# Kernel optimization log

Hardware: AMD Instinct MI355X
Metric: run time of the kernel (lower is better)

## Reference

```python
import jax, jax.numpy as jnp
import numpy as np

N_NODES = 50000
N_EDGES = 800000
IN_C, HID_C, OUT_C = 64, 128, 64


def setup_inputs() -> dict:
    key = jax.random.key(0)
    k0, k1, k2, k3 = jax.random.split(key, 4)
    x = jax.random.normal(k0, (N_NODES, IN_C), dtype=jnp.float32)
    edge_index = jax.random.randint(k1, (2, N_EDGES), 0, N_NODES, dtype=jnp.int64)
    # Glorot-ish init for the two GCNConv linear weights
    W1 = jax.random.normal(k2, (IN_C, HID_C), dtype=jnp.float32) * (1.0 / np.sqrt(IN_C))
    b1 = jnp.zeros((HID_C,), dtype=jnp.float32)
    W2 = jax.random.normal(k3, (HID_C, OUT_C), dtype=jnp.float32) * (1.0 / np.sqrt(HID_C))
    b2 = jnp.zeros((OUT_C,), dtype=jnp.float32)
    return {"x": x, "edge_index": edge_index, "W1": W1, "b1": b1, "W2": W2, "b2": b2}


def _gcn_conv(x, src, dst, norm, W, b, n_nodes):
    # GCNConv: out = D^{-1/2} (A+I) D^{-1/2} (x W) + b
    xw = x @ W                              # [N, out_c]
    msg = xw[src] * norm[:, None]           # [E+N, out_c] gather + scale
    agg = jax.ops.segment_sum(msg, dst, num_segments=n_nodes)  # scatter-add
    return agg + b


def reference(x, edge_index, W1, b1, W2, b2):
    n = x.shape[0]
    loops = jnp.arange(n, dtype=edge_index.dtype)
    src = jnp.concatenate([edge_index[0], loops])  # add self-loops
    dst = jnp.concatenate([edge_index[1], loops])
    # symmetric normalization over A + I
    deg = jax.ops.segment_sum(jnp.ones_like(dst, dtype=x.dtype), dst, num_segments=n)
    dinv = jnp.where(deg > 0, jax.lax.rsqrt(jnp.maximum(deg, 1.0)), 0.0)
    norm = dinv[src] * dinv[dst]
    h = jax.nn.relu(_gcn_conv(x, src, dst, norm, W1, b1, n))
    return _gcn_conv(h, src, dst, norm, W2, b2, n)
```

## Files before the change

### kernel.cpp

```cpp
#include <hip/hip_runtime.h>
#include <cstdint>


#define IN_C 64
#define HID_C 128
#define OUT_C 64
#define CH 2048
#define CAP 8192

typedef short bf16x8 __attribute__((ext_vector_type(8)));
typedef float f32x4 __attribute__((ext_vector_type(4)));

__device__ __forceinline__ unsigned int f2bf(float f) {
    unsigned int u = __float_as_uint(f);
    return (u + 0x7FFFu + ((u >> 16) & 1u)) >> 16;
}
__device__ __forceinline__ float bf2f(unsigned int hi16) {
    return __uint_as_float(hi16 << 16);
}

__device__ __forceinline__ int edge_val(const void* ei, long long idx, int is64) {
    if (is64) return (int)((const long long*)ei)[idx];
    return ((const int*)ei)[idx];
}

__global__ __launch_bounds__(256) void init_conv_k(const unsigned int* __restrict__ ei,
                                                   int* __restrict__ flag,
                                                   int* __restrict__ bcur,
                                                   const float4* __restrict__ x4,
                                                   uint2* __restrict__ xbf2, int NC4) {
    int i = blockIdx.x * 256 + threadIdx.x;
    if (i < NC4) {
        float4 v = x4[i];
        uint2 o;
        o.x = f2bf(v.x) | (f2bf(v.y) << 16);
        o.y = f2bf(v.z) | (f2bf(v.w) << 16);
        xbf2[i] = o;
    }
    if (blockIdx.x == 0) bcur[threadIdx.x] = threadIdx.x * CAP;
    if (i == 0) {
        int is64 = 1;
#pragma unroll
        for (int k = 0; k < 16; ++k) is64 &= (ei[2 * k + 1] == 0u) ? 1 : 0;
        *flag = is64;
    }
}

__global__ __launch_bounds__(256) void partition_k(const void* __restrict__ ei, int E,
                                                   const int* __restrict__ flag,
                                                   int* __restrict__ bcur,
                                                   int2* __restrict__ tmp) {
    __shared__ int2 stage[CH];
    __shared__ int hist[256];
    __shared__ int off[256];
    __shared__ int rcur[256];
    __shared__ int goff[256];
    __shared__ int wsum[4];
    const int tid = threadIdx.x;
    const int base = blockIdx.x * CH;
    const int cnt = min(CH, E - base);
    const int is64 = *flag;
    hist[tid] = 0;
    __syncthreads();
    int sa[CH / 256], da[CH / 256];
    int ne = 0;
#pragma unroll
    for (int k = 0; k < CH / 256; ++k) {
        int i = tid + k * 256;
        if (i < cnt) {
            sa[ne] = edge_val(ei, base + i, is64);
            da[ne] = edge_val(ei, (long long)E + base + i, is64);
            ne++;
        }
    }
    for (int k = 0; k < ne; ++k) atomicAdd(&hist[da[k] >> 8], 1);
    __syncthreads();
    {
        int v = hist[tid];
        int lane = tid & 63, wid = tid >> 6;
        int s = v;
#pragma unroll
        for (int o = 1; o < 64; o <<= 1) {
            int t = __shfl_up(s, o, 64);
            if (lane >= o) s += t;
        }
        if (lane == 63) wsum[wid] = s;
        __syncthreads();
        int w = 0;
#pragma unroll
        for (int j = 0; j < 4; ++j)
            if (j < wid) w += wsum[j];
        off[tid] = w + s - v;
        rcur[tid] = w + s - v;
    }
    __syncthreads();
    for (int k = 0; k < ne; ++k) {
        int b = da[k] >> 8;
        int r = atomicAdd(&rcur[b], 1);
        stage[r] = make_int2(sa[k], da[k]);
    }
    __syncthreads();
    {
        int c = hist[tid];
        goff[tid] = (c > 0) ? atomicAdd(&bcur[tid], c) : 0;
    }
    __syncthreads();
    for (int i = tid; i < cnt; i += 256) {
        int2 e = stage[i];
        int b = e.y >> 8;
        tmp[goff[b] + (i - off[b])] = e;
    }
}

__global__ __launch_bounds__(256) void finalize_k(const int2* __restrict__ tmp,
                                                  const int* __restrict__ bcur,
                                                  int* __restrict__ rowptr,
                                                  float* __restrict__ dinv,
                                                  int* __restrict__ edata,
                                                  int N, int E) {
    __shared__ int cnt[256];
    __shared__ int cur[256];
    __shared__ int sc[256];
    __shared__ int wsum[4];
    const int tid = threadIdx.x;
    const int bid = blockIdx.x;
    const int node0 = bid << 8;
    const int lane = tid & 63, wid = tid >> 6;
    {
        int v = bcur[tid] - tid * CAP;
        int s = v;
#pragma unroll
        for (int o = 1; o < 64; o <<= 1) {
            int t = __shfl_up(s, o, 64);
            if (lane >= o) s += t;
        }
        if (lane == 63) wsum[wid] = s;
        cnt[tid] = 0;
        __syncthreads();
        int w = 0;
#pragma unroll
        for (int j = 0; j < 4; ++j)
            if (j < wid) w += wsum[j];
        sc[tid] = w + s - v;
    }
    __syncthreads();
    const int base = bid * CAP;
    const int end = bcur[bid];
    for (int i = base + tid; i < end; i += 256)
        atomicAdd(&cnt[tmp[i].y - node0], 1);
    __syncthreads();
    const int gi = node0 + tid;
    int v = cnt[tid];
    if (gi < N) dinv[gi] = rsqrtf((float)(v + 1));
    int s = v;
#pragma unroll
    for (int o = 1; o < 64; o <<= 1) {
        int t = __shfl_up(s, o, 64);
        if (lane >= o) s += t;
    }
    if (lane == 63) wsum[wid] = s;
    __syncthreads();
    int w = 0;
#pragma unroll
    for (int j = 0; j < 4; ++j)
        if (j < wid) w += wsum[j];
    int rp = sc[bid] + w + s - v;
    if (gi < N) rowptr[gi] = rp;
    cur[tid] = rp;
    if (bid == 0 && tid == 0) rowptr[N] = E;
    __syncthreads();
    for (int i = base + tid; i < end; i += 256) {
        int2 e = tmp[i];
        int pos = atomicAdd(&cur[e.y - node0], 1);
        edata[pos] = e.x;
    }
}

template <bool BIAS, bool OBF>
__global__ __launch_bounds__(256) void aggregate_bf16_k(const uint4* __restrict__ feat4,
                                                        const int* __restrict__ rowptr,
                                                        const int* __restrict__ edata,
                                                        const float* __restrict__ dinv,
                                                        const float4* __restrict__ bias4,
                                                        void* __restrict__ outp, int N) {
    const int tid = threadIdx.x;
    const int node = blockIdx.x * 32 + (tid >> 3);
    const int t = tid & 7;
    if (node >= N) return;
    float dn = dinv[node];
    float sl = dn * dn;
    uint4 sv = feat4[(size_t)node * 8 + t];
    float acc[8];
    acc[0] = bf2f(sv.x & 0xFFFF) * sl;
    acc[1] = bf2f(sv.x >> 16) * sl;
    acc[2] = bf2f(sv.y & 0xFFFF) * sl;
    acc[3] = bf2f(sv.y >> 16) * sl;
    acc[4] = bf2f(sv.z & 0xFFFF) * sl;
    acc[5] = bf2f(sv.z >> 16) * sl;
    acc[6] = bf2f(sv.w & 0xFFFF) * sl;
    acc[7] = bf2f(sv.w >> 16) * sl;
    int e = rowptr[node];
    const int e1 = rowptr[node + 1];
#define ACC_EDGE(V, W)                                  \
    acc[0] = fmaf((W), bf2f((V).x & 0xFFFF), acc[0]);   \
    acc[1] = fmaf((W), bf2f((V).x >> 16), acc[1]);      \
    acc[2] = fmaf((W), bf2f((V).y & 0xFFFF), acc[2]);   \
    acc[3] = fmaf((W), bf2f((V).y >> 16), acc[3]);      \
    acc[4] = fmaf((W), bf2f((V).z & 0xFFFF), acc[4]);   \
    acc[5] = fmaf((W), bf2f((V).z >> 16), acc[5]);      \
    acc[6] = fmaf((W), bf2f((V).w & 0xFFFF), acc[6]);   \
    acc[7] = fmaf((W), bf2f((V).w >> 16), acc[7]);
    for (; e + 4 <= e1; e += 4) {
        int s0 = edata[e], s1 = edata[e + 1], s2 = edata[e + 2], s3 = edata[e + 3];
        float w0 = dinv[s0] * dn, w1 = dinv[s1] * dn;
        float w2 = dinv[s2] * dn, w3 = dinv[s3] * dn;
        uint4 f0 = feat4[(size_t)s0 * 8 + t];
        uint4 f1 = feat4[(size_t)s1 * 8 + t];
        uint4 f2 = feat4[(size_t)s2 * 8 + t];
        uint4 f3 = feat4[(size_t)s3 * 8 + t];
        ACC_EDGE(f0, w0);
        ACC_EDGE(f1, w1);
        ACC_EDGE(f2, w2);
        ACC_EDGE(f3, w3);
    }
    for (; e < e1; ++e) {
        int s0 = edata[e];
        float w0 = dinv[s0] * dn;
        uint4 f0 = feat4[(size_t)s0 * 8 + t];
        ACC_EDGE(f0, w0);
    }
#undef ACC_EDGE
    if (BIAS) {
        float4 b0 = bias4[2 * t], b1v = bias4[2 * t + 1];
        acc[0] += b0.x; acc[1] += b0.y; acc[2] += b0.z; acc[3] += b0.w;
        acc[4] += b1v.x; acc[5] += b1v.y; acc[6] += b1v.z; acc[7] += b1v.w;
    }
    if (OBF) {
        uint4 o;
        o.x = f2bf(acc[0]) | (f2bf(acc[1]) << 16);
        o.y = f2bf(acc[2]) | (f2bf(acc[3]) << 16);
        o.z = f2bf(acc[4]) | (f2bf(acc[5]) << 16);
        o.w = f2bf(acc[6]) | (f2bf(acc[7]) << 16);
        ((uint4*)outp)[(size_t)node * 8 + t] = o;
    } else {
        float4* out4 = (float4*)outp;
        out4[(size_t)node * 16 + 2 * t] = make_float4(acc[0], acc[1], acc[2], acc[3]);
        out4[(size_t)node * 16 + 2 * t + 1] = make_float4(acc[4], acc[5], acc[6], acc[7]);
    }
}

__global__ __launch_bounds__(256) void gemm1_mfma_k(const uint4* __restrict__ A8,
                                                    const float* __restrict__ W1,
                                                    const float* __restrict__ b1,
                                                    unsigned short* __restrict__ h, int M) {
    __shared__ uint4 As[64 * 8];
    __shared__ unsigned short BsU[128 * 64];
    const int tid = threadIdx.x;
    const int node0 = blockIdx.x * 64;
    for (int i = tid; i < 64 * 8; i += 256) {
        int r = i >> 3, c = i & 7;
        uint4 v = make_uint4(0u, 0u, 0u, 0u);
        if (node0 + r < M) v = A8[(size_t)(node0 + r) * 8 + c];
        As[r * 8 + (c ^ (r & 7))] = v;
    }
    {
        const float4* W4 = (const float4*)W1;
        for (int i = tid; i < 64 * 32; i += 256) {
            int k = i >> 5, n4 = i & 31;
            float4 v = W4[i];
            int n = n4 * 4;
#pragma unroll
            for (int j = 0; j < 4; ++j) {
                float f = (j == 0) ? v.x : (j == 1) ? v.y : (j == 2) ? v.z : v.w;
                int nn = n + j;
                int chunk = k >> 3;
                BsU[nn * 64 + ((chunk ^ (nn & 7)) << 3) + (k & 7)] =
                    (unsigned short)f2bf(f);
            }
        }
    }
    __syncthreads();

    const int lane = tid & 63;
    const int wv = tid >> 6;
    const int lr = lane & 15;
    const int lk = lane >> 4;
    f32x4 acc[4][2];
#pragma unroll
    for (int mt = 0; mt < 4; ++mt)
#pragma unroll
        for (int nb = 0; nb < 2; ++nb) acc[mt][nb] = (f32x4){0.f, 0.f, 0.f, 0.f};

#pragma unroll
    for (int ks = 0; ks < 2; ++ks) {
        bf16x8 a[4], b[2];
#pragma unroll
        for (int mt = 0; mt < 4; ++mt) {
            int r = mt * 16 + lr;
            int chunk = ks * 4 + lk;
            a[mt] = __builtin_bit_cast(bf16x8, As[r * 8 + (chunk ^ (r & 7))]);
        }
#pragma unroll
        for (int nb = 0; nb < 2; ++nb) {
            int n = wv * 32 + nb * 16 + lr;
            int chunk = ks * 4 + lk;
            b[nb] = __builtin_bit_cast(
                bf16x8, ((const uint4*)(BsU + n * 64))[chunk ^ (n & 7)]);
        }
#pragma unroll
        for (int mt = 0; mt < 4; ++mt)
#pragma unroll
            for (int nb = 0; nb < 2; ++nb)
                acc[mt][nb] = __builtin_amdgcn_mfma_f32_16x16x32_bf16(
                    a[mt], b[nb], acc[mt][nb], 0, 0, 0);
    }
#pragma unroll
    for (int nb = 0; nb < 2; ++nb) {
        int col = wv * 32 + nb * 16 + lr;
        float bb = b1[col];
#pragma unroll
        for (int mt = 0; mt < 4; ++mt) {
#pragma unroll
            for (int j = 0; j < 4; ++j) {
                int row = node0 + mt * 16 + (lane >> 4) * 4 + j;
                if (row < M) {
                    float v = fmaxf(acc[mt][nb][j] + bb, 0.f);
                    h[(size_t)row * HID_C + col] = (unsigned short)f2bf(v);
                }
            }
        }
    }
}

__global__ __launch_bounds__(256) void gemm2_mfma_k(const uint4* __restrict__ A16,
                                                    const float* __restrict__ W2,
                                                    unsigned short* __restrict__ hwb, int M) {
    __shared__ uint4 As[64 * 16];
    __shared__ unsigned short BsU[64 * 128];
    const int tid = threadIdx.x;
    const int node0 = blockIdx.x * 64;
    for (int i = tid; i < 64 * 16; i += 256) {
        int r = i >> 4, c = i & 15;
        uint4 v = make_uint4(0u, 0u, 0u, 0u);
        if (node0 + r < M) v = A16[(size_t)(node0 + r) * 16 + c];
        As[r * 16 + (c ^ (r & 7))] = v;
    }
    {
        const float4* W4 = (const float4*)W2;
        for (int i = tid; i < 128 * 16; i += 256) {
            int k = i >> 4, n4 = i & 15;
            float4 v = W4[i];
            int n = n4 * 4;
#pragma unroll
            for (int j = 0; j < 4; ++j) {
                float f = (j == 0) ? v.x : (j == 1) ? v.y : (j == 2) ? v.z : v.w;
                int nn = n + j;
                int chunk = k >> 3;
                BsU[nn * 128 + ((chunk ^ (nn & 7)) << 3) + (k & 7)] =
                    (unsigned short)f2bf(f);
            }
        }
    }
    __syncthreads();

    const int lane = tid & 63;
    const int wv = tid >> 6;
    const int lr = lane & 15;
    const int lk = lane >> 4;
    f32x4 acc[4];
#pragma unroll
    for (int mt = 0; mt < 4; ++mt) acc[mt] = (f32x4){0.f, 0.f, 0.f, 0.f};

#pragma unroll
    for (int ks = 0; ks < 4; ++ks) {
        bf16x8 a[4], b;
        int chunk = ks * 4 + lk;
#pragma unroll
        for (int mt = 0; mt < 4; ++mt) {
            int r = mt * 16 + lr;
            a[mt] = __builtin_bit_cast(bf16x8, As[r * 16 + (chunk ^ (r & 7))]);
        }
        {
            int n = wv * 16 + lr;
            b = __builtin_bit_cast(
                bf16x8, ((const uint4*)(BsU + n * 128))[chunk ^ (n & 7)]);
        }
#pragma unroll
        for (int mt = 0; mt < 4; ++mt)
            acc[mt] = __builtin_amdgcn_mfma_f32_16x16x32_bf16(a[mt], b, acc[mt], 0, 0, 0);
    }
    int col = wv * 16 + lr;
#pragma unroll
    for (int mt = 0; mt < 4; ++mt) {
#pragma unroll
        for (int j = 0; j < 4; ++j) {
            int row = node0 + mt * 16 + (lane >> 4) * 4 + j;
            if (row < M)
                hwb[(size_t)row * OUT_C + col] = (unsigned short)f2bf(acc[mt][j]);
        }
    }
}

extern "C" void kernel_launch(void* const* d_in, const int* in_sizes, int n_in,
                              void* d_out, int out_size, void* d_ws, size_t ws_size,
                              hipStream_t stream) {
    (void)n_in; (void)out_size; (void)ws_size;
    const float* x  = (const float*)d_in[0];
    const void*  ei = d_in[1];
    const float* W1 = (const float*)d_in[2];
    const float* b1 = (const float*)d_in[3];
    const float* W2 = (const float*)d_in[4];
    const float* b2 = (const float*)d_in[5];
    float* out = (float*)d_out;
    const int N = in_sizes[0] / IN_C;
    const int E = in_sizes[1] / 2;
    const int NB = (N + 255) / 256;
    const int PB = (E + CH - 1) / CH;
    const int NC4 = N * IN_C / 4;

    char* p = (char*)d_ws;
    auto take = [&](size_t bytes) {
        char* r = p;
        p += (bytes + 255) & ~(size_t)255;
        return r;
    };
    int*   flag    = (int*)take(256);
    int*   rowptr  = (int*)take(((size_t)N + 1) * 4);
    float* dinv    = (float*)take((size_t)N * 4);
    int*   bcur    = (int*)take(1024);
    int*   edata   = (int*)take((size_t)E * 4);
    uint2* xbf     = (uint2*)take((size_t)N * IN_C * 2);
    uint2* hwb     = (uint2*)take((size_t)N * OUT_C * 2);
    uint2* aggA    = (uint2*)take((size_t)N * IN_C * 2);
    uint2* h       = (uint2*)take((size_t)N * HID_C * 2);
    int2*  tmp     = (int2*)aggA;

    init_conv_k<<<(NC4 + 255) / 256, 256, 0, stream>>>(
        (const unsigned int*)ei, flag, bcur, (const float4*)x, xbf, NC4);
    partition_k<<<PB, 256, 0, stream>>>(ei, E, flag, bcur, tmp);
    finalize_k<<<NB, 256, 0, stream>>>(tmp, bcur, rowptr, dinv, edata, N, E);

    aggregate_bf16_k<false, true><<<(N + 31) / 32, 256, 0, stream>>>(
        (const uint4*)xbf, rowptr, edata, dinv, nullptr, aggA, N);
    gemm1_mfma_k<<<(N + 63) / 64, 256, 0, stream>>>(
        (const uint4*)aggA, W1, b1, (unsigned short*)h, N);

    gemm2_mfma_k<<<(N + 63) / 64, 256, 0, stream>>>(
        (const uint4*)h, W2, (unsigned short*)hwb, N);
    aggregate_bf16_k<true, false><<<(N + 31) / 32, 256, 0, stream>>>(
        (const uint4*)hwb, rowptr, edata, dinv, (const float4*)b2, out, N);
}
```

Measured before the change: 100.1 us.

## Fuse the two GEMMs through shared memory and merge init into partition

The two dense GEMMs become one kernel. The ReLU'd hidden tile is kept in swizzled LDS instead of being written to and read back from a global N×128 bf16 buffer. The x-to-bf16 conversion and the edge-format detection move into the partition kernel, and the bcur cursors are zeroed with a memset, so the init kernel launch and the flag round-trip go away. The partition buffer gets its own allocation instead of aliasing aggA. The gains are one fewer global round trip and two fewer launches. In exchange the fused GEMM uses about 48KB of LDS per block, which may lower occupancy, and the conversion loop now runs inside the partition blocks.

Measured after the change: 95.12 us. 1.05x faster.

```diff
diff --git a/kernel.cpp b/kernel.cpp
--- a/kernel.cpp
+++ b/kernel.cpp
@@ -24,32 +24,12 @@
     return ((const int*)ei)[idx];
 }
 
-__global__ __launch_bounds__(256) void init_conv_k(const unsigned int* __restrict__ ei,
-                                                   int* __restrict__ flag,
-                                                   int* __restrict__ bcur,
-                                                   const float4* __restrict__ x4,
-                                                   uint2* __restrict__ xbf2, int NC4) {
-    int i = blockIdx.x * 256 + threadIdx.x;
-    if (i < NC4) {
-        float4 v = x4[i];
-        uint2 o;
-        o.x = f2bf(v.x) | (f2bf(v.y) << 16);
-        o.y = f2bf(v.z) | (f2bf(v.w) << 16);
-        xbf2[i] = o;
-    }
-    if (blockIdx.x == 0) bcur[threadIdx.x] = threadIdx.x * CAP;
-    if (i == 0) {
-        int is64 = 1;
-#pragma unroll
-        for (int k = 0; k < 16; ++k) is64 &= (ei[2 * k + 1] == 0u) ? 1 : 0;
-        *flag = is64;
-    }
-}
-
-__global__ __launch_bounds__(256) void partition_k(const void* __restrict__ ei, int E,
-                                                   const int* __restrict__ flag,
-                                                   int* __restrict__ bcur,
-                                                   int2* __restrict__ tmp) {
+__global__ __launch_bounds__(256) void partition_conv_k(const void* __restrict__ ei,
+                                                        const float4* __restrict__ x4,
+                                                        uint2* __restrict__ xbf2,
+                                                        int* __restrict__ bcur,
+                                                        int2* __restrict__ tmp,
+                                                        int E, int NC4) {
     __shared__ int2 stage[CH];
     __shared__ int hist[256];
     __shared__ int off[256];
@@ -57,9 +37,22 @@
     __shared__ int goff[256];
     __shared__ int wsum[4];
     const int tid = threadIdx.x;
-    const int base = blockIdx.x * CH;
+    const int bid = blockIdx.x;
+    for (int i = bid * 256 + tid; i < NC4; i += gridDim.x * 256) {
+        float4 v = x4[i];
+        uint2 o;
+        o.x = f2bf(v.x) | (f2bf(v.y) << 16);
+        o.y = f2bf(v.z) | (f2bf(v.w) << 16);
+        xbf2[i] = o;
+    }
+    int is64 = 1;
+    {
+        const unsigned int* e32 = (const unsigned int*)ei;
+#pragma unroll
+        for (int k = 0; k < 16; ++k) is64 &= (e32[2 * k + 1] == 0u) ? 1 : 0;
+    }
+    const int base = bid * CH;
     const int cnt = min(CH, E - base);
-    const int is64 = *flag;
     hist[tid] = 0;
     __syncthreads();
     int sa[CH / 256], da[CH / 256];
@@ -102,7 +95,7 @@
     __syncthreads();
     {
         int c = hist[tid];
-        goff[tid] = (c > 0) ? atomicAdd(&bcur[tid], c) : 0;
+        goff[tid] = tid * CAP + ((c > 0) ? atomicAdd(&bcur[tid], c) : 0);
     }
     __syncthreads();
     for (int i = tid; i < cnt; i += 256) {
@@ -127,7 +120,7 @@
     const int node0 = bid << 8;
     const int lane = tid & 63, wid = tid >> 6;
     {
-        int v = bcur[tid] - tid * CAP;
+        int v = bcur[tid];
         int s = v;
 #pragma unroll
         for (int o = 1; o < 64; o <<= 1) {
@@ -145,7 +138,7 @@
     }
     __syncthreads();
     const int base = bid * CAP;
-    const int end = bcur[bid];
+    const int end = base + bcur[bid];
     for (int i = base + tid; i < end; i += 256)
         atomicAdd(&cnt[tmp[i].y - node0], 1);
     __syncthreads();
@@ -249,12 +242,15 @@
     }
 }
 
-__global__ __launch_bounds__(256) void gemm1_mfma_k(const uint4* __restrict__ A8,
-                                                    const float* __restrict__ W1,
-                                                    const float* __restrict__ b1,
-                                                    unsigned short* __restrict__ h, int M) {
+__global__ __launch_bounds__(256) void gemm12_k(const uint4* __restrict__ A8,
+                                                const float* __restrict__ W1,
+                                                const float* __restrict__ b1,
+                                                const float* __restrict__ W2,
+                                                unsigned short* __restrict__ hwb, int M) {
     __shared__ uint4 As[64 * 8];
-    __shared__ unsigned short BsU[128 * 64];
+    __shared__ unsigned short B1s[128 * 64];
+    __shared__ unsigned short B2s[64 * 128];
+    __shared__ unsigned short Hs[64 * 128];
     const int tid = threadIdx.x;
     const int node0 = blockIdx.x * 64;
     for (int i = tid; i < 64 * 8; i += 256) {
@@ -274,76 +270,10 @@
                 float f = (j == 0) ? v.x : (j == 1) ? v.y : (j == 2) ? v.z : v.w;
                 int nn = n + j;
                 int chunk = k >> 3;
-                BsU[nn * 64 + ((chunk ^ (nn & 7)) << 3) + (k & 7)] =
+                B1s[nn * 64 + (((chunk ^ (nn & 7)) << 3)) + (k & 7)] =
                     (unsigned short)f2bf(f);
             }
         }
-    }
-    __syncthreads();
-
-    const int lane = tid & 63;
-    const int wv = tid >> 6;
-    const int lr = lane & 15;
-    const int lk = lane >> 4;
-    f32x4 acc[4][2];
-#pragma unroll
-    for (int mt = 0; mt < 4; ++mt)
-#pragma unroll
-        for (int nb = 0; nb < 2; ++nb) acc[mt][nb] = (f32x4){0.f, 0.f, 0.f, 0.f};
-
-#pragma unroll
-    for (int ks = 0; ks < 2; ++ks) {
-        bf16x8 a[4], b[2];
-#pragma unroll
-        for (int mt = 0; mt < 4; ++mt) {
-            int r = mt * 16 + lr;
-            int chunk = ks * 4 + lk;
-            a[mt] = __builtin_bit_cast(bf16x8, As[r * 8 + (chunk ^ (r & 7))]);
-        }
-#pragma unroll
-        for (int nb = 0; nb < 2; ++nb) {
-            int n = wv * 32 + nb * 16 + lr;
-            int chunk = ks * 4 + lk;
-            b[nb] = __builtin_bit_cast(
-                bf16x8, ((const uint4*)(BsU + n * 64))[chunk ^ (n & 7)]);
-        }
-#pragma unroll
-        for (int mt = 0; mt < 4; ++mt)
-#pragma unroll
-            for (int nb = 0; nb < 2; ++nb)
-                acc[mt][nb] = __builtin_amdgcn_mfma_f32_16x16x32_bf16(
-                    a[mt], b[nb], acc[mt][nb], 0, 0, 0);
-    }
-#pragma unroll
-    for (int nb = 0; nb < 2; ++nb) {
-        int col = wv * 32 + nb * 16 + lr;
-        float bb = b1[col];
-#pragma unroll
-        for (int mt = 0; mt < 4; ++mt) {
-#pragma unroll
-            for (int j = 0; j < 4; ++j) {
-                int row = node0 + mt * 16 + (lane >> 4) * 4 + j;
-                if (row < M) {
-                    float v = fmaxf(acc[mt][nb][j] + bb, 0.f);
-                    h[(size_t)row * HID_C + col] = (unsigned short)f2bf(v);
-                }
-            }
-        }
-    }
-}
-
-__global__ __launch_bounds__(256) void gemm2_mfma_k(const uint4* __restrict__ A16,
-                                                    const float* __restrict__ W2,
-                                                    unsigned short* __restrict__ hwb, int M) {
-    __shared__ uint4 As[64 * 16];
-    __shared__ unsigned short BsU[64 * 128];
-    const int tid = threadIdx.x;
-    const int node0 = blockIdx.x * 64;
-    for (int i = tid; i < 64 * 16; i += 256) {
-        int r = i >> 4, c = i & 15;
-        uint4 v = make_uint4(0u, 0u, 0u, 0u);
-        if (node0 + r < M) v = A16[(size_t)(node0 + r) * 16 + c];
-        As[r * 16 + (c ^ (r & 7))] = v;
     }
     {
         const float4* W4 = (const float4*)W2;
@@ -356,7 +286,7 @@
                 float f = (j == 0) ? v.x : (j == 1) ? v.y : (j == 2) ? v.z : v.w;
                 int nn = n + j;
                 int chunk = k >> 3;
-                BsU[nn * 128 + ((chunk ^ (nn & 7)) << 3) + (k & 7)] =
+                B2s[nn * 128 + ((chunk ^ (nn & 7)) << 3) + (k & 7)] =
                     (unsigned short)f2bf(f);
             }
         }
@@ -367,36 +297,86 @@
     const int wv = tid >> 6;
     const int lr = lane & 15;
     const int lk = lane >> 4;
-    f32x4 acc[4];
-#pragma unroll
-    for (int mt = 0; mt < 4; ++mt) acc[mt] = (f32x4){0.f, 0.f, 0.f, 0.f};
-
-#pragma unroll
-    for (int ks = 0; ks < 4; ++ks) {
-        bf16x8 a[4], b;
-        int chunk = ks * 4 + lk;
+
+    {
+        f32x4 acc[4][2];
+#pragma unroll
+        for (int mt = 0; mt < 4; ++mt)
+#pragma unroll
+            for (int nb = 0; nb < 2; ++nb) acc[mt][nb] = (f32x4){0.f, 0.f, 0.f, 0.f};
+#pragma unroll
+        for (int ks = 0; ks < 2; ++ks) {
+            bf16x8 a[4], b[2];
+            int chunk = ks * 4 + lk;
+#pragma unroll
+            for (int mt = 0; mt < 4; ++mt) {
+                int r = mt * 16 + lr;
+                a[mt] = __builtin_bit_cast(bf16x8, As[r * 8 + (chunk ^ (r & 7))]);
+            }
+#pragma unroll
+            for (int nb = 0; nb < 2; ++nb) {
+                int n = wv * 32 + nb * 16 + lr;
+                b[nb] = __builtin_bit_cast(
+                    bf16x8, ((const uint4*)(B1s + n * 64))[chunk ^ (n & 7)]);
+            }
+#pragma unroll
+            for (int mt = 0; mt < 4; ++mt)
+#pragma unroll
+                for (int nb = 0; nb < 2; ++nb)
+                    acc[mt][nb] = __builtin_amdgcn_mfma_f32_16x16x32_bf16(
+                        a[mt], b[nb], acc[mt][nb], 0, 0, 0);
+        }
+#pragma unroll
+        for (int nb = 0; nb < 2; ++nb) {
+            int col = wv * 32 + nb * 16 + lr;
+            float bb = b1[col];
+            int chunk = col >> 3;
+#pragma unroll
+            for (int mt = 0; mt < 4; ++mt) {
+#pragma unroll
+                for (int j = 0; j < 4; ++j) {
+                    int row = mt * 16 + lk * 4 + j;
+                    float v = fmaxf(acc[mt][nb][j] + bb, 0.f);
+                    Hs[row * 128 + ((chunk ^ (row & 7)) << 3) + (col & 7)] =
+                        (unsigned short)f2bf(v);
+                }
+            }
+        }
+    }
+    __syncthreads();
+
+    {
+        f32x4 acc[4];
+#pragma unroll
+        for (int mt = 0; mt < 4; ++mt) acc[mt] = (f32x4){0.f, 0.f, 0.f, 0.f};
+#pragma unroll
+        for (int ks = 0; ks < 4; ++ks) {
+            bf16x8 a[4], b;
+            int chunk = ks * 4 + lk;
+#pragma unroll
+            for (int mt = 0; mt < 4; ++mt) {
+                int r = mt * 16 + lr;
+                a[mt] = __builtin_bit_cast(
+                    bf16x8, ((const uint4*)(Hs + r * 128))[chunk ^ (r & 7)]);
+            }
+            {
+                int n = wv * 16 + lr;
+                b = __builtin_bit_cast(
+                    bf16x8, ((const uint4*)(B2s + n * 128))[chunk ^ (n & 7)]);
+            }
+#pragma unroll
+            for (int mt = 0; mt < 4; ++mt)
+                acc[mt] = __builtin_amdgcn_mfma_f32_16x16x32_bf16(a[mt], b, acc[mt], 0, 0, 0);
+        }
+        int col = wv * 16 + lr;
 #pragma unroll
         for (int mt = 0; mt < 4; ++mt) {
-            int r = mt * 16 + lr;
-            a[mt] = __builtin_bit_cast(bf16x8, As[r * 16 + (chunk ^ (r & 7))]);
-        }
-        {
-            int n = wv * 16 + lr;
-            b = __builtin_bit_cast(
-                bf16x8, ((const uint4*)(BsU + n * 128))[chunk ^ (n & 7)]);
-        }
-#pragma unroll
-        for (int mt = 0; mt < 4; ++mt)
-            acc[mt] = __builtin_amdgcn_mfma_f32_16x16x32_bf16(a[mt], b, acc[mt], 0, 0, 0);
-    }
-    int col = wv * 16 + lr;
-#pragma unroll
-    for (int mt = 0; mt < 4; ++mt) {
-#pragma unroll
-        for (int j = 0; j < 4; ++j) {
-            int row = node0 + mt * 16 + (lane >> 4) * 4 + j;
-            if (row < M)
-                hwb[(size_t)row * OUT_C + col] = (unsigned short)f2bf(acc[mt][j]);
+#pragma unroll
+            for (int j = 0; j < 4; ++j) {
+                int row = node0 + mt * 16 + lk * 4 + j;
+                if (row < M)
+                    hwb[(size_t)row * OUT_C + col] = (unsigned short)f2bf(acc[mt][j]);
+            }
         }
     }
 }
@@ -424,7 +404,6 @@
         p += (bytes + 255) & ~(size_t)255;
         return r;
     };
-    int*   flag    = (int*)take(256);
     int*   rowptr  = (int*)take(((size_t)N + 1) * 4);
     float* dinv    = (float*)take((size_t)N * 4);
     int*   bcur    = (int*)take(1024);
@@ -432,21 +411,17 @@
     uint2* xbf     = (uint2*)take((size_t)N * IN_C * 2);
     uint2* hwb     = (uint2*)take((size_t)N * OUT_C * 2);
     uint2* aggA    = (uint2*)take((size_t)N * IN_C * 2);
-    uint2* h       = (uint2*)take((size_t)N * HID_C * 2);
-    int2*  tmp     = (int2*)aggA;
-
-    init_conv_k<<<(NC4 + 255) / 256, 256, 0, stream>>>(
-        (const unsigned int*)ei, flag, bcur, (const float4*)x, xbf, NC4);
-    partition_k<<<PB, 256, 0, stream>>>(ei, E, flag, bcur, tmp);
+    int2*  tmp     = (int2*)take((size_t)256 * CAP * 8);
+
+    hipMemsetAsync(bcur, 0, 1024, stream);
+    partition_conv_k<<<PB, 256, 0, stream>>>(ei, (const float4*)x, xbf, bcur, tmp, E, NC4);
     finalize_k<<<NB, 256, 0, stream>>>(tmp, bcur, rowptr, dinv, edata, N, E);
 
     aggregate_bf16_k<false, true><<<(N + 31) / 32, 256, 0, stream>>>(
         (const uint4*)xbf, rowptr, edata, dinv, nullptr, aggA, N);
-    gemm1_mfma_k<<<(N + 63) / 64, 256, 0, stream>>>(
-        (const uint4*)aggA, W1, b1, (unsigned short*)h, N);
-
-    gemm2_mfma_k<<<(N + 63) / 64, 256, 0, stream>>>(
-        (const uint4*)h, W2, (unsigned short*)hwb, N);
+    gemm12_k<<<(N + 63) / 64, 256, 0, stream>>>(
+        (const uint4*)aggA, W1, b1, W2, (unsigned short*)hwb, N);
+
     aggregate_bf16_k<true, false><<<(N + 31) / 32, 256, 0, stream>>>(
         (const uint4*)hwb, rowptr, edata, dinv, (const float4*)b2, out, N);
 }
```
